# Kernel tuning notes

Measured on AMD Instinct MI355X. Metric: run time of the kernel, lower is better.

The kernel has to match this reference:

```python
import jax, jax.numpy as jnp
import numpy as np

B, IN_DIM, OUT_DIM, N_WIN, N_SEQ, N_REAL = 4, 8, 64, 64, 4096, 6144


def setup_inputs() -> dict:
    key = jax.random.key(0)
    k1, k2, k3, k4 = jax.random.split(key, 4)
    x = jax.random.normal(k1, (B, IN_DIM, N_SEQ), dtype=jnp.float32)
    bound = 1.0 / np.sqrt(IN_DIM * N_WIN)  # torch uniform init bound k=1/(inDim*nWin)
    weight = jax.random.uniform(k2, (OUT_DIM, IN_DIM, N_WIN), jnp.float32, -bound, bound)
    bias = jax.random.uniform(k3, (OUT_DIM,), jnp.float32, -bound, bound)
    # sorted, unique onset indices per batch (irregular but monotone, in-range)
    ks = jax.random.split(k4, B)
    sourceIdx = jax.vmap(
        lambda k: jnp.sort(jax.random.choice(k, N_REAL, (N_SEQ,), replace=False))
    )(ks).astype(jnp.int32)
    return {"x": x, "weight": weight, "bias": bias,
            "sourceIdx": sourceIdx, "nRealLen": N_REAL}


def reference(x, weight, bias, sourceIdx, nRealLen):
    # LTITRFGen (ifAddBiasInForward=False): broadcast-mul + sum over inDim
    # == einsum over the stimulus-feature axis.
    TRFs = jnp.einsum('bis,oiw->bows', x, weight)  # (B, outDim, nWin, nSeq)
    Bz, O, W, S = TRFs.shape

    # TRFAligner: scatter TRFs into zero cache at per-sample source indices
    def scatter_one(trf_b, idx_b):  # trf_b: (O, W, S), idx_b: (S,)
        return jnp.zeros((O, W, nRealLen), trf_b.dtype).at[:, :, idx_b].set(trf_b)

    cache = jax.vmap(scatter_one)(TRFs, sourceIdx)  # (B, O, W, nRealLen)

    # torch fold with kernel (nWin,1) == overlap-add along the lag axis:
    # out[b,o,t] = sum_w cache[b,o,w,t-w]
    out = jnp.zeros((Bz, O, nRealLen + W - 1), TRFs.dtype)
    for w in range(W):  # static small lag loop (nWin=64)
        out = out.at[:, :, w:w + nRealLen].add(cache[:, :, w])

    # crop to nRealLen and add per-channel LTI bias (ifEnableUserTRFGen=False path)
    return out[:, :, :nRealLen] + bias[None, :, None]
```

## Files before the change

kernel.cpp:

```cpp
#include <hip/hip_runtime.h>
#include <hip/hip_bf16.h>

#define BB 4
#define IN_DIM 8
#define OUT_DIM 64
#define N_WIN 64
#define N_SEQ 4096
#define N_REAL 6144

#define ZR 6208

typedef __attribute__((ext_vector_type(8)))  short short8;
typedef __attribute__((ext_vector_type(16))) float floatx16;

static __device__ __forceinline__ unsigned short f2bf(float f) {
    union { float f; unsigned int u; } v; v.f = f;
    unsigned int r = v.u + 0x7fffu + ((v.u >> 16) & 1u);
    return (unsigned short)(r >> 16);
}

__global__ __launch_bounds__(256) void k_zero(uint4* p, int n) {
    int i = blockIdx.x * 256 + threadIdx.x;
    if (i < n) p[i] = make_uint4(0u, 0u, 0u, 0u);
}

__global__ __launch_bounds__(256)
void k_prep(const float* __restrict__ x, const float* __restrict__ w,
            const int* __restrict__ sidx,
            unsigned short* __restrict__ w2, unsigned short* __restrict__ zf)
{
    const int bid = blockIdx.x, tid = threadIdx.x;
    if (bid < 64) {
        int tg = bid * 256 + tid;
        int b = tg >> 12, s = tg & 4095;
        int tau = sidx[b * N_SEQ + s];
        const float* xp = x + (size_t)b * IN_DIM * N_SEQ + s;
        unsigned short v[8];
        #pragma unroll
        for (int i = 0; i < 8; ++i) v[i] = f2bf(xp[(size_t)i * N_SEQ]);
        uint4 pk;
        pk.x = v[0] | (v[1] << 16); pk.y = v[2] | (v[3] << 16);
        pk.z = v[4] | (v[5] << 16); pk.w = v[6] | (v[7] << 16);
        *(uint4*)(zf + ((size_t)b * ZR + tau + 63) * 8) = pk;
    } else {
        int tg = (bid - 64) * 256 + tid;
        int l = tg & 63, o = tg >> 6;
        const float* wp = w + (size_t)o * IN_DIM * N_WIN + l;
        unsigned short v[8];
        #pragma unroll
        for (int i = 0; i < 8; ++i) v[i] = f2bf(wp[(size_t)i * N_WIN]);
        uint4 pk;
        pk.x = v[0] | (v[1] << 16); pk.y = v[2] | (v[3] << 16);
        pk.z = v[4] | (v[5] << 16); pk.w = v[6] | (v[7] << 16);
        *(uint4*)(w2 + ((size_t)l * OUT_DIM + o) * 8) = pk;
    }
}

__global__ __launch_bounds__(128)
void k_gemm(const unsigned short* __restrict__ w2,
            const unsigned short* __restrict__ zf,
            const float* __restrict__ bias, float* __restrict__ out)
{
    __shared__ unsigned short zlds[96 * 8];

    const int tid = threadIdx.x;
    const int t0  = blockIdx.x * 32;
    const int b   = blockIdx.y;

    if (tid < 96)
        *(uint4*)(zlds + tid * 8) =
            *(const uint4*)(zf + ((size_t)b * ZR + t0 + tid) * 8);
    __syncthreads();

    const int mh = tid >> 6;
    const int ln = tid & 31;
    const int lq = (tid >> 5) & 1;

    floatx16 acc = {};
    const short8* wv = (const short8*)w2;
    const short8* zv = (const short8*)zlds;

    #pragma unroll 8
    for (int ks = 0; ks < 32; ++ks) {
        const int l = 2 * ks + lq;
        short8 a = wv[l * OUT_DIM + mh * 32 + ln];
        short8 bz = zv[ln + 63 - l];
        acc = __builtin_amdgcn_mfma_f32_32x32x16_bf16(a, bz, acc, 0, 0, 0);
    }

    #pragma unroll
    for (int p = 0; p < 16; ++p) {
        int o = (p & 3) + 8 * (p >> 2) + 4 * lq + mh * 32;
        out[((size_t)b * OUT_DIM + o) * N_REAL + t0 + ln] = acc[p] + bias[o];
    }
}

extern "C" void kernel_launch(void* const* d_in, const int* in_sizes, int n_in,
                              void* d_out, int out_size, void* d_ws, size_t ws_size,
                              hipStream_t stream) {
    const float* px = nullptr; const float* pw = nullptr;
    const float* pb = nullptr; const int* ps = nullptr;

    for (int i = 0; i < n_in; ++i) {
        switch (in_sizes[i]) {
            case BB * IN_DIM * N_SEQ:        px = (const float*)d_in[i]; break;
            case OUT_DIM * IN_DIM * N_WIN:   pw = (const float*)d_in[i]; break;
            case OUT_DIM:                    pb = (const float*)d_in[i]; break;
            case BB * N_SEQ:                 ps = (const int*)d_in[i];   break;
            default: break;
        }
    }
    if (!px || !pw || !pb || !ps) {
        px = (const float*)d_in[0]; pw = (const float*)d_in[1];
        pb = (const float*)d_in[2]; ps = (const int*)d_in[3];
    }

    unsigned short* w2 = (unsigned short*)d_ws;
    unsigned short* zf = w2 + N_WIN * OUT_DIM * IN_DIM;
    float* out = (float*)d_out;

    const int zf_u4 = BB * ZR * IN_DIM / 8;
    k_zero<<<(zf_u4 + 255) / 256, 256, 0, stream>>>((uint4*)zf, zf_u4);
    k_prep<<<80, 256, 0, stream>>>(px, pw, ps, w2, zf);
    k_gemm<<<dim3(N_REAL / 32, BB), 128, 0, stream>>>(w2, zf, pb, out);
}
```

Before: 74.47 us.

## Fuse zero, prep and GEMM kernels into one cooperative kernel with grid sync

Replaces the three separate launches (zero-fill, bf16 prep/scatter, MFMA GEMM) with a single cooperative kernel. The scatter becomes a gather: each thread binary-searches the sorted source indices to decide whether its padded slot holds data or zero, so the separate zeroing pass goes away. A grid-wide sync separates the prep phase from the GEMM phase. This removes launch overhead between kernels, but adds a cooperative launch, a grid barrier across 768 blocks, and a 12-step binary search per slot.

```diff
diff --git a/kernel.cpp b/kernel.cpp
--- a/kernel.cpp
+++ b/kernel.cpp
@@ -1,5 +1,8 @@
 #include <hip/hip_runtime.h>
+#include <hip/hip_cooperative_groups.h>
 #include <hip/hip_bf16.h>
+
+namespace cg = cooperative_groups;
 
 #define BB 4
 #define IN_DIM 8
@@ -19,53 +22,56 @@
     return (unsigned short)(r >> 16);
 }
 
-__global__ __launch_bounds__(256) void k_zero(uint4* p, int n) {
-    int i = blockIdx.x * 256 + threadIdx.x;
-    if (i < n) p[i] = make_uint4(0u, 0u, 0u, 0u);
-}
+__global__ __launch_bounds__(128)
+void k_fused(const float* __restrict__ x, const float* __restrict__ w,
+             const float* __restrict__ bias, const int* __restrict__ sidx,
+             unsigned short* __restrict__ w2, unsigned short* __restrict__ zf,
+             float* __restrict__ out)
+{
+    __shared__ unsigned short zlds[96 * 8];
 
-__global__ __launch_bounds__(256)
-void k_prep(const float* __restrict__ x, const float* __restrict__ w,
-            const int* __restrict__ sidx,
-            unsigned short* __restrict__ w2, unsigned short* __restrict__ zf)
-{
-    const int bid = blockIdx.x, tid = threadIdx.x;
-    if (bid < 64) {
-        int tg = bid * 256 + tid;
-        int b = tg >> 12, s = tg & 4095;
-        int tau = sidx[b * N_SEQ + s];
-        const float* xp = x + (size_t)b * IN_DIM * N_SEQ + s;
-        unsigned short v[8];
-        #pragma unroll
-        for (int i = 0; i < 8; ++i) v[i] = f2bf(xp[(size_t)i * N_SEQ]);
-        uint4 pk;
-        pk.x = v[0] | (v[1] << 16); pk.y = v[2] | (v[3] << 16);
-        pk.z = v[4] | (v[5] << 16); pk.w = v[6] | (v[7] << 16);
-        *(uint4*)(zf + ((size_t)b * ZR + tau + 63) * 8) = pk;
-    } else {
-        int tg = (bid - 64) * 256 + tid;
-        int l = tg & 63, o = tg >> 6;
+    const int tid = threadIdx.x;
+    const int bx  = blockIdx.x;
+    const int by  = blockIdx.y;
+    const int g   = (by * 192 + bx) * 128 + tid;
+
+    if (g < BB * ZR) {
+        const int b   = g / ZR;
+        const int q   = g - b * ZR;
+        const int tau = q - 63;
+        uint4 pk = make_uint4(0u, 0u, 0u, 0u);
+        if ((unsigned)tau < (unsigned)N_REAL) {
+            const int* idxb = sidx + b * N_SEQ;
+            int lo = 0, hi = N_SEQ;
+            while (lo < hi) { int m = (lo + hi) >> 1; if (idxb[m] < tau) lo = m + 1; else hi = m; }
+            if (lo < N_SEQ && idxb[lo] == tau) {
+                const float* xp = x + (size_t)b * IN_DIM * N_SEQ + lo;
+                unsigned short v[8];
+                #pragma unroll
+                for (int i = 0; i < 8; ++i) v[i] = f2bf(xp[(size_t)i * N_SEQ]);
+                pk.x = v[0] | ((unsigned)v[1] << 16); pk.y = v[2] | ((unsigned)v[3] << 16);
+                pk.z = v[4] | ((unsigned)v[5] << 16); pk.w = v[6] | ((unsigned)v[7] << 16);
+            }
+        }
+        *(uint4*)(zf + (size_t)g * 8) = pk;
+    } else if (g < BB * ZR + OUT_DIM * N_WIN) {
+        const int tg = g - BB * ZR;
+        const int l = tg & 63, o = tg >> 6;
         const float* wp = w + (size_t)o * IN_DIM * N_WIN + l;
         unsigned short v[8];
         #pragma unroll
         for (int i = 0; i < 8; ++i) v[i] = f2bf(wp[(size_t)i * N_WIN]);
         uint4 pk;
-        pk.x = v[0] | (v[1] << 16); pk.y = v[2] | (v[3] << 16);
-        pk.z = v[4] | (v[5] << 16); pk.w = v[6] | (v[7] << 16);
+        pk.x = v[0] | ((unsigned)v[1] << 16); pk.y = v[2] | ((unsigned)v[3] << 16);
+        pk.z = v[4] | ((unsigned)v[5] << 16); pk.w = v[6] | ((unsigned)v[7] << 16);
         *(uint4*)(w2 + ((size_t)l * OUT_DIM + o) * 8) = pk;
     }
-}
 
-__global__ __launch_bounds__(128)
-void k_gemm(const unsigned short* __restrict__ w2,
-            const unsigned short* __restrict__ zf,
-            const float* __restrict__ bias, float* __restrict__ out)
-{
-    __shared__ unsigned short zlds[96 * 8];
+    __threadfence();
+    cg::this_grid().sync();
 
-    const int tid = threadIdx.x;
-    const int t0  = blockIdx.x * 32;
-    const int b   = blockIdx.y;
+    const int t0 = bx * 32;
+    const int b  = by;
 
     if (tid < 96)
         *(uint4*)(zlds + tid * 8) =
@@ -83,7 +89,7 @@
     #pragma unroll 8
     for (int ks = 0; ks < 32; ++ks) {
         const int l = 2 * ks + lq;
-        short8 a = wv[l * OUT_DIM + mh * 32 + ln];
+        short8 a  = wv[l * OUT_DIM + mh * 32 + ln];
         short8 bz = zv[ln + 63 - l];
         acc = __builtin_amdgcn_mfma_f32_32x32x16_bf16(a, bz, acc, 0, 0, 0);
     }
@@ -119,8 +125,8 @@
     unsigned short* zf = w2 + N_WIN * OUT_DIM * IN_DIM;
     float* out = (float*)d_out;
 
-    const int zf_u4 = BB * ZR * IN_DIM / 8;
-    k_zero<<<(zf_u4 + 255) / 256, 256, 0, stream>>>((uint4*)zf, zf_u4);
-    k_prep<<<80, 256, 0, stream>>>(px, pw, ps, w2, zf);
-    k_gemm<<<dim3(N_REAL / 32, BB), 128, 0, stream>>>(w2, zf, pb, out);
+    void* args[] = { (void*)&px, (void*)&pw, (void*)&pb, (void*)&ps,
+                     (void*)&w2, (void*)&zf, (void*)&out };
+    hipLaunchCooperativeKernel((const void*)k_fused, dim3(192, BB), dim3(128),
+                               args, 0, stream);
 }
```

New measurement: 205.0 us. 175% more time.
